# Performance work log

Hardware: AMD Instinct MI355X
Metric: run time of the kernel (lower is better)

Reference implementation:

```python
import jax, jax.numpy as jnp
import numpy as np

VOCAB_SIZE = 43
N_LABELS = VOCAB_SIZE + 2  # 45
START_IDX = N_LABELS - 2   # 43
STOP_IDX = N_LABELS - 1    # 44
NEG_INF = -10000.0


def setup_inputs() -> dict:
    key = jax.random.key(0)
    k1, k2, k3 = jax.random.split(key, 3)
    B, S = 1024, 512
    logits = jax.random.normal(k1, (B, S, N_LABELS), dtype=jnp.float32)
    # lengths in [1, S]
    lens = jax.random.randint(k2, (B,), 1, S + 1, dtype=jnp.int32)
    # learned CRF transition matrix, transitions[i, j] = score of j -> i
    transitions = jax.random.normal(k3, (N_LABELS, N_LABELS), dtype=jnp.float32)
    return {"logits": logits, "lens": lens, "transitions": transitions}


def reference(logits, lens, transitions):
    """CRF forward algorithm (log partition function), matching CRF.forward.

    logits: [B, S, L] emission scores
    lens:   [B] int lengths
    transitions: [L, L] with transitions[i, j] = score(prev=j -> cur=i)
    returns norm: [B] log partition score per sequence.
    """
    B = logits.shape[0]
    alpha0 = jnp.full((B, N_LABELS), NEG_INF, dtype=logits.dtype)
    alpha0 = alpha0.at[:, START_IDX].set(0.0)

    def step(carry, logit_t):
        alpha, c_lens = carry
        # mat[b, i, j] = transitions[i, j] + alpha[b, j] + logit_t[b, i]
        # alpha_nxt[b, i] = logit_t[b, i] + LSE_j(transitions[i, j] + alpha[b, j])
        mat = transitions[None, :, :] + alpha[:, None, :]          # [B, L, L]
        alpha_nxt = logit_t + jax.nn.logsumexp(mat, axis=2)        # [B, L]
        active = (c_lens > 0)[:, None]                             # [B, 1]
        alpha = jnp.where(active, alpha_nxt, alpha)
        return (alpha, c_lens - 1), None

    logits_t = jnp.swapaxes(logits, 0, 1)  # [S, B, L]
    (alpha, _), _ = jax.lax.scan(step, (alpha0, lens), logits_t)
    alpha = alpha + transitions[STOP_IDX][None, :]
    norm = jax.nn.logsumexp(alpha, axis=1)  # [B]
    return norm
```

## Files before the change

kernel.cpp:

```cpp
#include <hip/hip_runtime.h>
#include <math.h>

#define NL 45
#define START_IDX 43
#define STOP_IDX 44

#define FOR45(F) \
  F(0) F(1) F(2) F(3) F(4) F(5) F(6) F(7) F(8) F(9) \
  F(10) F(11) F(12) F(13) F(14) F(15) F(16) F(17) F(18) F(19) \
  F(20) F(21) F(22) F(23) F(24) F(25) F(26) F(27) F(28) F(29) \
  F(30) F(31) F(32) F(33) F(34) F(35) F(36) F(37) F(38) F(39) \
  F(40) F(41) F(42) F(43) F(44)

__device__ __forceinline__ float wave_max64(float v) {
    v = fmaxf(v, __shfl_xor(v, 32, 64));
    v = fmaxf(v, __shfl_xor(v, 16, 64));
    v = fmaxf(v, __shfl_xor(v, 8, 64));
    v = fmaxf(v, __shfl_xor(v, 4, 64));
    v = fmaxf(v, __shfl_xor(v, 2, 64));
    v = fmaxf(v, __shfl_xor(v, 1, 64));
    return v;
}

__device__ __forceinline__ float wave_sum64(float v) {
    v += __shfl_xor(v, 32, 64);
    v += __shfl_xor(v, 16, 64);
    v += __shfl_xor(v, 8, 64);
    v += __shfl_xor(v, 4, 64);
    v += __shfl_xor(v, 2, 64);
    v += __shfl_xor(v, 1, 64);
    return v;
}

__global__ __attribute__((amdgpu_flat_work_group_size(64, 64),
                          amdgpu_waves_per_eu(1, 1)))
void crf_fwd_kernel(
        const float* __restrict__ logits,
        const int* __restrict__ lens,
        const float* __restrict__ trans,
        float* __restrict__ out,
        int S) {
    const int b = blockIdx.x;
    const int lane = threadIdx.x;
    const bool real = lane < NL;
    const int rl = real ? lane : 0;

#define E_DECL(J) float e##J = real ? __expf(trans[rl * NL + (J)]) : 0.0f;
    FOR45(E_DECL)
#undef E_DECL
    asm volatile("" : "+v"(e0), "+v"(e1), "+v"(e2), "+v"(e3), "+v"(e4),
                      "+v"(e5), "+v"(e6), "+v"(e7), "+v"(e8), "+v"(e9),
                      "+v"(e10), "+v"(e11), "+v"(e12), "+v"(e13), "+v"(e14),
                      "+v"(e15), "+v"(e16), "+v"(e17), "+v"(e18), "+v"(e19),
                      "+v"(e20), "+v"(e21), "+v"(e22));
    asm volatile("" : "+v"(e23), "+v"(e24), "+v"(e25), "+v"(e26), "+v"(e27),
                      "+v"(e28), "+v"(e29), "+v"(e30), "+v"(e31), "+v"(e32),
                      "+v"(e33), "+v"(e34), "+v"(e35), "+v"(e36), "+v"(e37),
                      "+v"(e38), "+v"(e39), "+v"(e40), "+v"(e41), "+v"(e42),
                      "+v"(e43), "+v"(e44));

    const float tstop = trans[STOP_IDX * NL + rl];
    const int len = lens[b];

    float q = (real && lane == START_IDX) ? 1.0f : 0.0f;
    int esum = 0;

    const float* lp = logits + (size_t)b * (size_t)S * NL + rl;
    const int tmax = S - 1;

#define LD(T) lp[(size_t)(((T) < tmax) ? (T) : tmax) * NL]
    float f0 = LD(0), f1 = LD(1), f2 = LD(2), f3 = LD(3);
    float p0 = LD(4), p1 = LD(5), p2 = LD(6), p3 = LD(7);

#define RDL(J) const float qb##J = __uint_as_float( \
        __builtin_amdgcn_readlane(__float_as_uint(q), (J)));
#define MACJ(J) acc[(J) & 3] = fmaf(e##J, qb##J, acc[(J) & 3]);
#define STEP(K) { \
        const float el = __expf(f##K); \
        FOR45(RDL) \
        __builtin_amdgcn_sched_barrier(0); \
        float acc[4] = {0.0f, 0.0f, 0.0f, 0.0f}; \
        FOR45(MACJ) \
        const float qn = el * ((acc[0] + acc[1]) + (acc[2] + acc[3])); \
        q = (t0 + (K) < len) ? qn : q; \
    }

    for (int t0 = 0; t0 < len; t0 += 4) {
        const float n0 = LD(t0 + 8), n1 = LD(t0 + 9);
        const float n2 = LD(t0 + 10), n3 = LD(t0 + 11);

        STEP(0) STEP(1) STEP(2) STEP(3)

        const float mq = wave_max64(q);
        int ex; (void)frexpf(mq, &ex);
        q = ldexpf(q, -ex);
        esum += ex;

        f0 = p0; f1 = p1; f2 = p2; f3 = p3;
        p0 = n0; p1 = n1; p2 = n2; p3 = n3;
    }
#undef STEP
#undef MACJ
#undef RDL
#undef LD

    const float a = __logf(q) + tstop;
    const float mm = wave_max64(a);
    const float e = __expf(a - mm);
    const float ssum = wave_sum64(e);
    if (lane == 0) {
        const float M = (float)esum * 0.69314718055994531f;
        out[b] = M + mm + __logf(ssum);
    }
}

extern "C" void kernel_launch(void* const* d_in, const int* in_sizes, int n_in,
                              void* d_out, int out_size, void* d_ws, size_t ws_size,
                              hipStream_t stream) {
    const float* logits = (const float*)d_in[0];
    const int* lens = (const int*)d_in[1];
    const float* trans = (const float*)d_in[2];
    float* out = (float*)d_out;

    const int B = in_sizes[1];
    const int S = in_sizes[0] / (B * NL);

    crf_fwd_kernel<<<B, 64, 0, stream>>>(logits, lens, trans, out, S);
}
```

Baseline: 234.2 us.

## Split CRF reduction over four waves with LDS partial-sum exchange

```diff
diff --git a/kernel.cpp b/kernel.cpp
--- a/kernel.cpp
+++ b/kernel.cpp
@@ -5,12 +5,7 @@
 #define START_IDX 43
 #define STOP_IDX 44
 
-#define FOR45(F) \
-  F(0) F(1) F(2) F(3) F(4) F(5) F(6) F(7) F(8) F(9) \
-  F(10) F(11) F(12) F(13) F(14) F(15) F(16) F(17) F(18) F(19) \
-  F(20) F(21) F(22) F(23) F(24) F(25) F(26) F(27) F(28) F(29) \
-  F(30) F(31) F(32) F(33) F(34) F(35) F(36) F(37) F(38) F(39) \
-  F(40) F(41) F(42) F(43) F(44)
+#define FOR12(F) F(0) F(1) F(2) F(3) F(4) F(5) F(6) F(7) F(8) F(9) F(10) F(11)
 
 __device__ __forceinline__ float wave_max64(float v) {
     v = fmaxf(v, __shfl_xor(v, 32, 64));
@@ -32,8 +27,7 @@
     return v;
 }
 
-__global__ __attribute__((amdgpu_flat_work_group_size(64, 64),
-                          amdgpu_waves_per_eu(1, 1)))
+__global__ __launch_bounds__(256, 4)
 void crf_fwd_kernel(
         const float* __restrict__ logits,
         const int* __restrict__ lens,
@@ -41,76 +35,94 @@
         float* __restrict__ out,
         int S) {
     const int b = blockIdx.x;
-    const int lane = threadIdx.x;
+    const int tid = (int)threadIdx.x;
+    const int lane = tid & 63;
+    const int w = tid >> 6;
     const bool real = lane < NL;
     const int rl = real ? lane : 0;
 
-#define E_DECL(J) float e##J = real ? __expf(trans[rl * NL + (J)]) : 0.0f;
-    FOR45(E_DECL)
+    __shared__ float parts[2][4][64];
+    __shared__ __align__(16) int exps[2][4];
+
+#define E_DECL(J) const int j##J = 12 * w + (J); \
+    const float e##J = (real && j##J < NL) \
+        ? __expf(trans[rl * NL + ((j##J) < NL ? (j##J) : 0)]) : 0.0f;
+    FOR12(E_DECL)
 #undef E_DECL
-    asm volatile("" : "+v"(e0), "+v"(e1), "+v"(e2), "+v"(e3), "+v"(e4),
-                      "+v"(e5), "+v"(e6), "+v"(e7), "+v"(e8), "+v"(e9),
-                      "+v"(e10), "+v"(e11), "+v"(e12), "+v"(e13), "+v"(e14),
-                      "+v"(e15), "+v"(e16), "+v"(e17), "+v"(e18), "+v"(e19),
-                      "+v"(e20), "+v"(e21), "+v"(e22));
-    asm volatile("" : "+v"(e23), "+v"(e24), "+v"(e25), "+v"(e26), "+v"(e27),
-                      "+v"(e28), "+v"(e29), "+v"(e30), "+v"(e31), "+v"(e32),
-                      "+v"(e33), "+v"(e34), "+v"(e35), "+v"(e36), "+v"(e37),
-                      "+v"(e38), "+v"(e39), "+v"(e40), "+v"(e41), "+v"(e42),
-                      "+v"(e43), "+v"(e44));
 
     const float tstop = trans[STOP_IDX * NL + rl];
     const int len = lens[b];
 
     float q = (real && lane == START_IDX) ? 1.0f : 0.0f;
     int esum = 0;
+    int pa = 0;
 
     const float* lp = logits + (size_t)b * (size_t)S * NL + rl;
     const int tmax = S - 1;
-
 #define LD(T) lp[(size_t)(((T) < tmax) ? (T) : tmax) * NL]
     float f0 = LD(0), f1 = LD(1), f2 = LD(2), f3 = LD(3);
     float p0 = LD(4), p1 = LD(5), p2 = LD(6), p3 = LD(7);
 
 #define RDL(J) const float qb##J = __uint_as_float( \
-        __builtin_amdgcn_readlane(__float_as_uint(q), (J)));
+        __builtin_amdgcn_readlane(__float_as_uint(q), j##J));
 #define MACJ(J) acc[(J) & 3] = fmaf(e##J, qb##J, acc[(J) & 3]);
-#define STEP(K) { \
+#define MAXQ(J) { const unsigned u = __float_as_uint(qb##J); mx = (u > mx) ? u : mx; }
+
+#define STEP(K, RN) { \
         const float el = __expf(f##K); \
-        FOR45(RDL) \
+        FOR12(RDL) \
         __builtin_amdgcn_sched_barrier(0); \
         float acc[4] = {0.0f, 0.0f, 0.0f, 0.0f}; \
-        FOR45(MACJ) \
-        const float qn = el * ((acc[0] + acc[1]) + (acc[2] + acc[3])); \
+        FOR12(MACJ) \
+        parts[pa][w][lane] = (acc[0] + acc[1]) + (acc[2] + acc[3]); \
+        if (RN) { \
+            unsigned mx = __float_as_uint(qb0); \
+            MAXQ(1) MAXQ(2) MAXQ(3) MAXQ(4) MAXQ(5) MAXQ(6) MAXQ(7) \
+            MAXQ(8) MAXQ(9) MAXQ(10) MAXQ(11) \
+            if (lane == 0) exps[pa][w] = (int)mx; \
+        } \
+        __syncthreads(); \
+        const float Ssum = (parts[pa][0][lane] + parts[pa][1][lane]) \
+                         + (parts[pa][2][lane] + parts[pa][3][lane]); \
+        const float qn = el * Ssum; \
         q = (t0 + (K) < len) ? qn : q; \
+        if (RN) { \
+            const int4 ev = *((const int4*)exps[pa]); \
+            int m01 = (ev.x > ev.y) ? ev.x : ev.y; \
+            int m23 = (ev.z > ev.w) ? ev.z : ev.w; \
+            const int mex = (m01 > m23) ? m01 : m23; \
+            const int ex = (mex >> 23) - 127; \
+            q = ldexpf(q, -ex); \
+            esum += ex; \
+        } \
+        pa ^= 1; \
     }
 
+#pragma unroll 2
     for (int t0 = 0; t0 < len; t0 += 4) {
         const float n0 = LD(t0 + 8), n1 = LD(t0 + 9);
         const float n2 = LD(t0 + 10), n3 = LD(t0 + 11);
 
-        STEP(0) STEP(1) STEP(2) STEP(3)
-
-        const float mq = wave_max64(q);
-        int ex; (void)frexpf(mq, &ex);
-        q = ldexpf(q, -ex);
-        esum += ex;
+        STEP(0, 0) STEP(1, 0) STEP(2, 0) STEP(3, 1)
 
         f0 = p0; f1 = p1; f2 = p2; f3 = p3;
         p0 = n0; p1 = n1; p2 = n2; p3 = n3;
     }
 #undef STEP
+#undef MAXQ
 #undef MACJ
 #undef RDL
 #undef LD
 
-    const float a = __logf(q) + tstop;
-    const float mm = wave_max64(a);
-    const float e = __expf(a - mm);
-    const float ssum = wave_sum64(e);
-    if (lane == 0) {
-        const float M = (float)esum * 0.69314718055994531f;
-        out[b] = M + mm + __logf(ssum);
+    if (w == 0) {
+        const float a = __logf(q) + tstop;
+        const float mm = wave_max64(a);
+        const float e = __expf(a - mm);
+        const float ssum = wave_sum64(e);
+        if (lane == 0) {
+            const float M = (float)esum * 0.69314718055994531f;
+            out[b] = M + mm + __logf(ssum);
+        }
     }
 }
 
@@ -125,5 +137,5 @@
     const int B = in_sizes[1];
     const int S = in_sizes[0] / (B * NL);
 
-    crf_fwd_kernel<<<B, 64, 0, stream>>>(logits, lens, trans, out, S);
+    crf_fwd_kernel<<<B, 256, 0, stream>>>(logits, lens, trans, out, S);
 }
```

After: 328.6 us. +40.3%, slower.

## Interleave readlanes with FMAs and fold renormalization max into scalar readlanes

Applied to the files above, without the earlier changes.

```diff
diff --git a/kernel.cpp b/kernel.cpp
--- a/kernel.cpp
+++ b/kernel.cpp
@@ -4,13 +4,6 @@
 #define NL 45
 #define START_IDX 43
 #define STOP_IDX 44
-
-#define FOR45(F) \
-  F(0) F(1) F(2) F(3) F(4) F(5) F(6) F(7) F(8) F(9) \
-  F(10) F(11) F(12) F(13) F(14) F(15) F(16) F(17) F(18) F(19) \
-  F(20) F(21) F(22) F(23) F(24) F(25) F(26) F(27) F(28) F(29) \
-  F(30) F(31) F(32) F(33) F(34) F(35) F(36) F(37) F(38) F(39) \
-  F(40) F(41) F(42) F(43) F(44)
 
 __device__ __forceinline__ float wave_max64(float v) {
     v = fmaxf(v, __shfl_xor(v, 32, 64));
@@ -45,6 +38,13 @@
     const bool real = lane < NL;
     const int rl = real ? lane : 0;
 
+#define FOR45(F) \
+  F(0) F(1) F(2) F(3) F(4) F(5) F(6) F(7) F(8) F(9) \
+  F(10) F(11) F(12) F(13) F(14) F(15) F(16) F(17) F(18) F(19) \
+  F(20) F(21) F(22) F(23) F(24) F(25) F(26) F(27) F(28) F(29) \
+  F(30) F(31) F(32) F(33) F(34) F(35) F(36) F(37) F(38) F(39) \
+  F(40) F(41) F(42) F(43) F(44)
+
 #define E_DECL(J) float e##J = real ? __expf(trans[rl * NL + (J)]) : 0.0f;
     FOR45(E_DECL)
 #undef E_DECL
@@ -74,33 +74,60 @@
 
 #define RDL(J) const float qb##J = __uint_as_float( \
         __builtin_amdgcn_readlane(__float_as_uint(q), (J)));
-#define MACJ(J) acc[(J) & 3] = fmaf(e##J, qb##J, acc[(J) & 3]);
-#define STEP(K) { \
+#define INI(J) acc[(J) & 7] = e##J * qb##J;
+#define MAC(J) acc[(J) & 7] = fmaf(e##J, qb##J, acc[(J) & 7]);
+#define MXQ(J) { const unsigned u##J = __float_as_uint(qb##J); \
+                 mx = (u##J > mx) ? u##J : mx; }
+
+#define STEP(K, RN) { \
         const float el = __expf(f##K); \
-        FOR45(RDL) \
-        __builtin_amdgcn_sched_barrier(0); \
-        float acc[4] = {0.0f, 0.0f, 0.0f, 0.0f}; \
-        FOR45(MACJ) \
-        const float qn = el * ((acc[0] + acc[1]) + (acc[2] + acc[3])); \
+        float acc[8]; \
+        RDL(0) RDL(1) RDL(2) RDL(3) RDL(4) RDL(5) \
+        RDL(6) RDL(7) RDL(8) RDL(9) RDL(10) RDL(11) \
+        RDL(12) INI(0)  RDL(13) INI(1)  RDL(14) INI(2)  RDL(15) INI(3) \
+        RDL(16) INI(4)  RDL(17) INI(5)  RDL(18) INI(6)  RDL(19) INI(7) \
+        RDL(20) MAC(8)  RDL(21) MAC(9)  RDL(22) MAC(10) RDL(23) MAC(11) \
+        RDL(24) MAC(12) RDL(25) MAC(13) RDL(26) MAC(14) RDL(27) MAC(15) \
+        RDL(28) MAC(16) RDL(29) MAC(17) RDL(30) MAC(18) RDL(31) MAC(19) \
+        RDL(32) MAC(20) RDL(33) MAC(21) RDL(34) MAC(22) RDL(35) MAC(23) \
+        RDL(36) MAC(24) RDL(37) MAC(25) RDL(38) MAC(26) RDL(39) MAC(27) \
+        RDL(40) MAC(28) RDL(41) MAC(29) RDL(42) MAC(30) RDL(43) MAC(31) \
+        RDL(44) MAC(32) \
+        MAC(33) MAC(34) MAC(35) MAC(36) MAC(37) MAC(38) \
+        MAC(39) MAC(40) MAC(41) MAC(42) MAC(43) MAC(44) \
+        const float s01 = acc[0] + acc[1], s23 = acc[2] + acc[3]; \
+        const float s45 = acc[4] + acc[5], s67 = acc[6] + acc[7]; \
+        const float qn = el * ((s01 + s23) + (s45 + s67)); \
         q = (t0 + (K) < len) ? qn : q; \
+        if (RN) { \
+            unsigned mx = __float_as_uint(qb0); \
+            MXQ(1) MXQ(2) MXQ(3) MXQ(4) MXQ(5) MXQ(6) MXQ(7) MXQ(8) \
+            MXQ(9) MXQ(10) MXQ(11) MXQ(12) MXQ(13) MXQ(14) MXQ(15) \
+            MXQ(16) MXQ(17) MXQ(18) MXQ(19) MXQ(20) MXQ(21) MXQ(22) \
+            MXQ(23) MXQ(24) MXQ(25) MXQ(26) MXQ(27) MXQ(28) MXQ(29) \
+            MXQ(30) MXQ(31) MXQ(32) MXQ(33) MXQ(34) MXQ(35) MXQ(36) \
+            MXQ(37) MXQ(38) MXQ(39) MXQ(40) MXQ(41) MXQ(42) MXQ(43) \
+            MXQ(44) \
+            const int ex = (int)(mx >> 23) - 127; \
+            q = ldexpf(q, -ex); \
+            esum += ex; \
+        } \
     }
 
+#pragma unroll 2
     for (int t0 = 0; t0 < len; t0 += 4) {
         const float n0 = LD(t0 + 8), n1 = LD(t0 + 9);
         const float n2 = LD(t0 + 10), n3 = LD(t0 + 11);
 
-        STEP(0) STEP(1) STEP(2) STEP(3)
-
-        const float mq = wave_max64(q);
-        int ex; (void)frexpf(mq, &ex);
-        q = ldexpf(q, -ex);
-        esum += ex;
+        STEP(0, 0) STEP(1, 0) STEP(2, 0) STEP(3, 1)
 
         f0 = p0; f1 = p1; f2 = p2; f3 = p3;
         p0 = n0; p1 = n1; p2 = n2; p3 = n3;
     }
 #undef STEP
-#undef MACJ
+#undef MXQ
+#undef MAC
+#undef INI
 #undef RDL
 #undef LD
 
```

Measured after the change: 262.0 us. 11.9% more time.
